# Kernel optimization log

Measured on AMD Instinct MI355X. Metric: run time of the kernel, lower is better.

Reference implementation:

```python
import jax, jax.numpy as jnp
import numpy as np

B, D, P, E, C = 2048, 4096, 64, 8, 64
K = D // P  # conv kernel = stride = input_dim / patch_num


def setup_inputs() -> dict:
    key = jax.random.key(0)
    k1, k2, k3, k4 = jax.random.split(key, 4)
    x = jax.random.normal(k1, (B, 1, D), jnp.float32)
    router_w = jax.random.normal(k2, (E, K), jnp.float32) * 0.02   # Router conv weight [E,1,K] squeezed
    expert_w = jax.random.normal(k3, (E, 2 * C, K), jnp.float32) * 0.001  # per-expert conv weights (small=True scaling)
    expert_b = jax.random.normal(k4, (E, 2 * C), jnp.float32) * 0.001
    return {"x": x, "router_w": router_w, "expert_w": expert_w, "expert_b": expert_b}


def reference(x, router_w, expert_w, expert_b):
    b, _, d = x.shape
    e, k = router_w.shape
    p = d // k
    c = expert_w.shape[1] // 2

    # Conv1d(1, ch, K, stride=K) == per-patch matmul; sum over dim 2 == sum over patches.
    patches = x.reshape(b, p, k)                                   # [B,P,K]

    # Router (eval mode: no noise)
    select = jnp.einsum('bpk,ek->be', patches, router_w)           # [B,E]

    # top1 routing
    gate = jnp.max(select, axis=-1)                                # [B]
    index = jnp.argmax(select, axis=-1)                            # [B]
    onehot = jax.nn.one_hot(index, e, dtype=select.dtype)          # [B,E]

    # aux load-balance loss
    density = onehot.mean(axis=0)
    density_proxy = select.mean(axis=0)
    loss = (density_proxy * density).mean() * float(e ** 2)

    # combine/dispatch (mask_flat is all ones for top1)
    combine = gate[:, None] * onehot                               # [B,E]
    dispatch = jax.lax.stop_gradient((combine != 0).astype(select.dtype))  # bool cast detaches grad
    select0 = dispatch

    # Dense dispatch: every expert sees the full batch, zero-masked by dispatch.
    # z[e,b,c,p] = conv of (dispatch[b,e]*x[b]) with expert e's kernel, + bias
    z = jnp.einsum('bpk,eck->ebcp', patches, expert_w)             # [E,B,2C,P]
    z = z * dispatch.T[:, :, None, None] + expert_b[:, None, :, None]
    z = z ** 3                                                     # nonlinear=True
    s = z.sum(axis=-1)                                             # sum over patches -> [E,B,2C]
    expert_out = jnp.stack([s[..., :c].sum(-1), s[..., c:].sum(-1)], axis=-1)  # [E,B,2]

    out = jnp.einsum('be,ebl->bl', combine, expert_out)            # [B,2]
    out = jax.nn.softmax(out, axis=1)
    return out, select0, loss
```

## Files before the change

### kernel.cpp

```cpp
#include <hip/hip_runtime.h>

#define BB 2048
#define DD 4096
#define PP 64
#define KK 64
#define EE 8
#define C2 128

typedef __attribute__((ext_vector_type(8))) short short8;
typedef __attribute__((ext_vector_type(4))) float floatx4;

__device__ inline unsigned short f2bf(float f) {
    unsigned int u = __builtin_bit_cast(unsigned int, f);
    u += 0x7FFFu + ((u >> 16) & 1u);
    return (unsigned short)(u >> 16);
}

__global__ __launch_bounds__(256) void moe_fused(
    const float* __restrict__ x, const float* __restrict__ rw,
    const float* __restrict__ ew, const float* __restrict__ eb,
    float* __restrict__ out, float* __restrict__ ws_sel)
{
    __shared__ __align__(16) unsigned short patb[64][72];
    __shared__ __align__(16) unsigned char ubuf[128 * 72 * 2];
    __shared__ float biasf[128];
    __shared__ float red0[4], red1[4];
    __shared__ float gate_s;
    __shared__ int idx_s;

    float (*cpart)[64]         = (float (*)[64])ubuf;
    unsigned short (*wbf)[72]  = (unsigned short (*)[72])ubuf;

    const int b = blockIdx.x;
    const int tid = threadIdx.x;

    {
        const float4* xb4 = (const float4*)(x + (size_t)b * DD);
        float c0 = 0.f, c1 = 0.f, c2 = 0.f, c3 = 0.f;
        #pragma unroll
        for (int j = 0; j < 4; ++j) {
            int idx = j * 256 + tid;
            float4 v = xb4[idx];
            int p = idx >> 4;
            int k = (idx & 15) << 2;
            ushort4 w4;
            w4.x = f2bf(v.x); w4.y = f2bf(v.y);
            w4.z = f2bf(v.z); w4.w = f2bf(v.w);
            *(ushort4*)&patb[p][k] = w4;
            c0 += v.x; c1 += v.y; c2 += v.z; c3 += v.w;
        }
        int m  = tid >> 4;
        int kq = (tid & 15) << 2;
        float4 cp; cp.x = c0; cp.y = c1; cp.z = c2; cp.w = c3;
        *(float4*)&cpart[m][kq] = cp;
    }
    __syncthreads();

    if (tid < 64) {
        float s = 0.f;
        #pragma unroll
        for (int m2 = 0; m2 < 16; ++m2) s += cpart[m2][tid];
        float myg = 0.f; int myix = 0;
        #pragma unroll
        for (int e2 = 0; e2 < 8; ++e2) {
            float d = s * rw[e2 * KK + tid];
            d += __shfl_xor(d, 32); d += __shfl_xor(d, 16); d += __shfl_xor(d, 8);
            d += __shfl_xor(d, 4);  d += __shfl_xor(d, 2);  d += __shfl_xor(d, 1);
            if (tid == e2) ws_sel[b * 8 + e2] = d;
            if (e2 == 0 || d > myg) { myg = d; myix = e2; }
        }
        if (tid == 0) { gate_s = myg; idx_s = myix; }
        if (tid < 8)
            out[BB * 2 + b * 8 + tid] = (tid == myix && myg != 0.f) ? 1.f : 0.f;
    }
    __syncthreads();

    const int e = idx_s;
    const float gate = gate_s;

    {
        const float4* we4 = (const float4*)(ew + (size_t)e * (C2 * KK));
        #pragma unroll
        for (int j = 0; j < 8; ++j) {
            int idx = j * 256 + tid;
            float4 v = we4[idx];
            int c = idx >> 4;
            int k = (idx & 15) << 2;
            ushort4 w4;
            w4.x = f2bf(v.x); w4.y = f2bf(v.y);
            w4.z = f2bf(v.z); w4.w = f2bf(v.w);
            *(ushort4*)&wbf[c][k] = w4;
        }
        if (tid < 128) biasf[tid] = eb[e * C2 + tid];
    }
    __syncthreads();

    const int w = tid >> 6;
    const int lane = tid & 63;
    const int r = lane & 15;
    const int q = lane >> 4;

    floatx4 acc[8];
    #pragma unroll
    for (int nt = 0; nt < 8; ++nt) acc[nt] = (floatx4){0.f, 0.f, 0.f, 0.f};

    #pragma unroll
    for (int kb = 0; kb < 2; ++kb) {
        const int k0 = kb * 32 + q * 8;
        short8 a = *(const short8*)&patb[w * 16 + r][k0];
        #pragma unroll
        for (int nt = 0; nt < 8; ++nt) {
            short8 bfr = *(const short8*)&wbf[nt * 16 + r][k0];
            acc[nt] = __builtin_amdgcn_mfma_f32_16x16x32_bf16(a, bfr, acc[nt], 0, 0, 0);
        }
    }

    float h0 = 0.f, h1 = 0.f;
    #pragma unroll
    for (int nt = 0; nt < 8; ++nt) {
        float bs = biasf[nt * 16 + r];
        #pragma unroll
        for (int i = 0; i < 4; ++i) {
            float z = acc[nt][i] + bs;
            float z3 = z * z * z;
            if (nt < 4) h0 += z3; else h1 += z3;
        }
    }
    #pragma unroll
    for (int off = 32; off > 0; off >>= 1) {
        h0 += __shfl_down(h0, off);
        h1 += __shfl_down(h1, off);
    }
    if (lane == 0) { red0[w] = h0; red1[w] = h1; }
    __syncthreads();
    if (tid == 0) {
        float t0 = red0[0] + red0[1] + red0[2] + red0[3];
        float t1 = red1[0] + red1[1] + red1[2] + red1[3];
        float l0 = gate * t0, l1 = gate * t1;
        float m = fmaxf(l0, l1);
        float e0 = __expf(l0 - m), e1 = __expf(l1 - m);
        float inv = 1.f / (e0 + e1);
        out[b * 2 + 0] = e0 * inv;
        out[b * 2 + 1] = e1 * inv;
    }
}

__global__ __launch_bounds__(256) void loss_kernel(
    const float* __restrict__ ws_sel, float* __restrict__ out)
{
    __shared__ float red[4][16];
    const int t = threadIdx.x;
    const int w = t >> 6, lane = t & 63;

    float p[8] = {0,0,0,0,0,0,0,0};
    float c[8] = {0,0,0,0,0,0,0,0};
    #pragma unroll
    for (int it = 0; it < BB / 256; ++it) {
        int b = it * 256 + t;
        const float4* row = (const float4*)(ws_sel + b * 8);
        float4 r0 = row[0], r1 = row[1];
        float v[8] = {r0.x, r0.y, r0.z, r0.w, r1.x, r1.y, r1.z, r1.w};
        float g = v[0]; int ix = 0;
        #pragma unroll
        for (int e2 = 1; e2 < 8; ++e2)
            if (v[e2] > g) { g = v[e2]; ix = e2; }
        #pragma unroll
        for (int e2 = 0; e2 < 8; ++e2) p[e2] += v[e2];
        c[ix] += 1.f;
    }
    #pragma unroll
    for (int off = 32; off > 0; off >>= 1) {
        #pragma unroll
        for (int e2 = 0; e2 < 8; ++e2) {
            p[e2] += __shfl_xor(p[e2], off);
            c[e2] += __shfl_xor(c[e2], off);
        }
    }
    if (lane == 0) {
        #pragma unroll
        for (int e2 = 0; e2 < 8; ++e2) { red[w][e2] = p[e2]; red[w][8 + e2] = c[e2]; }
    }
    __syncthreads();
    if (t == 0) {
        float loss = 0.f;
        #pragma unroll
        for (int e2 = 0; e2 < 8; ++e2) {
            float sp = red[0][e2] + red[1][e2] + red[2][e2] + red[3][e2];
            float sc = red[0][8 + e2] + red[1][8 + e2] + red[2][8 + e2] + red[3][8 + e2];
            loss += (sp / (float)BB) * (sc / (float)BB);
        }
        out[BB * 2 + BB * 8] = loss * (float)EE;
    }
}

extern "C" void kernel_launch(void* const* d_in, const int* in_sizes, int n_in,
                              void* d_out, int out_size, void* d_ws, size_t ws_size,
                              hipStream_t stream) {
    (void)in_sizes; (void)n_in; (void)out_size; (void)ws_size;
    const float* x  = (const float*)d_in[0];
    const float* rw = (const float*)d_in[1];
    const float* ew = (const float*)d_in[2];
    const float* eb = (const float*)d_in[3];
    float* out = (float*)d_out;
    float* ws  = (float*)d_ws;
    moe_fused<<<BB, 256, 0, stream>>>(x, rw, ew, eb, out, ws);
    loss_kernel<<<1, 256, 0, stream>>>(ws, out);
}
```

Before: 93.49 us.

## Map one sample per wavefront and pre-convert expert weights to bf16

Reworks the MoE kernel so that each 64-lane wavefront handles one batch row in registers, with four rows per block. This removes shared-memory staging and block-level barriers. Expert weights are converted to bf16 once by a separate prep kernel into workspace, and each wave then loads its selected expert's weight fragments straight from global memory. Activations are truncated rather than rounded to bf16, which slightly changes numerics, and the change adds one more kernel launch.

```diff
diff --git a/kernel.cpp b/kernel.cpp
--- a/kernel.cpp
+++ b/kernel.cpp
@@ -15,133 +15,118 @@
     u += 0x7FFFu + ((u >> 16) & 1u);
     return (unsigned short)(u >> 16);
 }
+__device__ inline unsigned pack2_trunc(float lo, float hi) {
+    unsigned ul = __builtin_bit_cast(unsigned, lo);
+    unsigned uh = __builtin_bit_cast(unsigned, hi);
+    return (uh & 0xFFFF0000u) | (ul >> 16);
+}
 
-__global__ __launch_bounds__(256) void moe_fused(
+__global__ __launch_bounds__(256) void prep_w(const float* __restrict__ ew,
+                                              unsigned short* __restrict__ wbf) {
+    int idx = blockIdx.x * 256 + threadIdx.x;
+    float4 v = ((const float4*)ew)[idx];
+    ushort4 o;
+    o.x = f2bf(v.x); o.y = f2bf(v.y); o.z = f2bf(v.z); o.w = f2bf(v.w);
+    ((ushort4*)wbf)[idx] = o;
+}
+
+__global__ __launch_bounds__(256) void moe3(
     const float* __restrict__ x, const float* __restrict__ rw,
-    const float* __restrict__ ew, const float* __restrict__ eb,
+    const unsigned short* __restrict__ wbf, const float* __restrict__ eb,
     float* __restrict__ out, float* __restrict__ ws_sel)
 {
-    __shared__ __align__(16) unsigned short patb[64][72];
-    __shared__ __align__(16) unsigned char ubuf[128 * 72 * 2];
-    __shared__ float biasf[128];
-    __shared__ float red0[4], red1[4];
-    __shared__ float gate_s;
-    __shared__ int idx_s;
+    const int lane = threadIdx.x & 63;
+    const int b = blockIdx.x * 4 + (threadIdx.x >> 6);
+    const int r = lane & 15, q = lane >> 4;
+    const float* xb = x + (size_t)b * DD;
 
-    float (*cpart)[64]         = (float (*)[64])ubuf;
-    unsigned short (*wbf)[72]  = (unsigned short (*)[72])ubuf;
-
-    const int b = blockIdx.x;
-    const int tid = threadIdx.x;
-
-    {
-        const float4* xb4 = (const float4*)(x + (size_t)b * DD);
-        float c0 = 0.f, c1 = 0.f, c2 = 0.f, c3 = 0.f;
+    float ps[16];
+    #pragma unroll
+    for (int j = 0; j < 16; ++j) ps[j] = 0.f;
+    short8 af[8];
+    #pragma unroll
+    for (int mt = 0; mt < 4; ++mt) {
         #pragma unroll
-        for (int j = 0; j < 4; ++j) {
-            int idx = j * 256 + tid;
-            float4 v = xb4[idx];
-            int p = idx >> 4;
-            int k = (idx & 15) << 2;
-            ushort4 w4;
-            w4.x = f2bf(v.x); w4.y = f2bf(v.y);
-            w4.z = f2bf(v.z); w4.w = f2bf(v.w);
-            *(ushort4*)&patb[p][k] = w4;
-            c0 += v.x; c1 += v.y; c2 += v.z; c3 += v.w;
-        }
-        int m  = tid >> 4;
-        int kq = (tid & 15) << 2;
-        float4 cp; cp.x = c0; cp.y = c1; cp.z = c2; cp.w = c3;
-        *(float4*)&cpart[m][kq] = cp;
-    }
-    __syncthreads();
-
-    if (tid < 64) {
-        float s = 0.f;
-        #pragma unroll
-        for (int m2 = 0; m2 < 16; ++m2) s += cpart[m2][tid];
-        float myg = 0.f; int myix = 0;
-        #pragma unroll
-        for (int e2 = 0; e2 < 8; ++e2) {
-            float d = s * rw[e2 * KK + tid];
-            d += __shfl_xor(d, 32); d += __shfl_xor(d, 16); d += __shfl_xor(d, 8);
-            d += __shfl_xor(d, 4);  d += __shfl_xor(d, 2);  d += __shfl_xor(d, 1);
-            if (tid == e2) ws_sel[b * 8 + e2] = d;
-            if (e2 == 0 || d > myg) { myg = d; myix = e2; }
-        }
-        if (tid == 0) { gate_s = myg; idx_s = myix; }
-        if (tid < 8)
-            out[BB * 2 + b * 8 + tid] = (tid == myix && myg != 0.f) ? 1.f : 0.f;
-    }
-    __syncthreads();
-
-    const int e = idx_s;
-    const float gate = gate_s;
-
-    {
-        const float4* we4 = (const float4*)(ew + (size_t)e * (C2 * KK));
-        #pragma unroll
-        for (int j = 0; j < 8; ++j) {
-            int idx = j * 256 + tid;
-            float4 v = we4[idx];
-            int c = idx >> 4;
-            int k = (idx & 15) << 2;
-            ushort4 w4;
-            w4.x = f2bf(v.x); w4.y = f2bf(v.y);
-            w4.z = f2bf(v.z); w4.w = f2bf(v.w);
-            *(ushort4*)&wbf[c][k] = w4;
-        }
-        if (tid < 128) biasf[tid] = eb[e * C2 + tid];
-    }
-    __syncthreads();
-
-    const int w = tid >> 6;
-    const int lane = tid & 63;
-    const int r = lane & 15;
-    const int q = lane >> 4;
-
-    floatx4 acc[8];
-    #pragma unroll
-    for (int nt = 0; nt < 8; ++nt) acc[nt] = (floatx4){0.f, 0.f, 0.f, 0.f};
-
-    #pragma unroll
-    for (int kb = 0; kb < 2; ++kb) {
-        const int k0 = kb * 32 + q * 8;
-        short8 a = *(const short8*)&patb[w * 16 + r][k0];
-        #pragma unroll
-        for (int nt = 0; nt < 8; ++nt) {
-            short8 bfr = *(const short8*)&wbf[nt * 16 + r][k0];
-            acc[nt] = __builtin_amdgcn_mfma_f32_16x16x32_bf16(a, bfr, acc[nt], 0, 0, 0);
+        for (int kb = 0; kb < 2; ++kb) {
+            const float* base = xb + (mt * 16 + r) * 64 + kb * 32 + q * 8;
+            float4 v0 = *(const float4*)base;
+            float4 v1 = *(const float4*)(base + 4);
+            ps[kb*8+0] += v0.x; ps[kb*8+1] += v0.y; ps[kb*8+2] += v0.z; ps[kb*8+3] += v0.w;
+            ps[kb*8+4] += v1.x; ps[kb*8+5] += v1.y; ps[kb*8+6] += v1.z; ps[kb*8+7] += v1.w;
+            uint4 u;
+            u.x = pack2_trunc(v0.x, v0.y); u.y = pack2_trunc(v0.z, v0.w);
+            u.z = pack2_trunc(v1.x, v1.y); u.w = pack2_trunc(v1.z, v1.w);
+            af[mt * 2 + kb] = __builtin_bit_cast(short8, u);
         }
     }
 
+    float d[8];
+    #pragma unroll
+    for (int e2 = 0; e2 < 8; ++e2) {
+        const float* rwe = rw + e2 * KK;
+        float4 a0 = *(const float4*)(rwe + q * 8);
+        float4 a1 = *(const float4*)(rwe + q * 8 + 4);
+        float4 b0 = *(const float4*)(rwe + 32 + q * 8);
+        float4 b1 = *(const float4*)(rwe + 32 + q * 8 + 4);
+        float t = ps[0]*a0.x + ps[1]*a0.y + ps[2]*a0.z + ps[3]*a0.w
+                + ps[4]*a1.x + ps[5]*a1.y + ps[6]*a1.z + ps[7]*a1.w
+                + ps[8]*b0.x + ps[9]*b0.y + ps[10]*b0.z + ps[11]*b0.w
+                + ps[12]*b1.x + ps[13]*b1.y + ps[14]*b1.z + ps[15]*b1.w;
+        t += __shfl_xor(t, 1);  t += __shfl_xor(t, 2);  t += __shfl_xor(t, 4);
+        t += __shfl_xor(t, 8);  t += __shfl_xor(t, 16); t += __shfl_xor(t, 32);
+        d[e2] = t;
+    }
+    float gate = d[0]; int e = 0;
+    #pragma unroll
+    for (int e2 = 1; e2 < 8; ++e2)
+        if (d[e2] > gate) { gate = d[e2]; e = e2; }
+
+    if (lane == 0) {
+        float4 s0 = make_float4(d[0], d[1], d[2], d[3]);
+        float4 s1 = make_float4(d[4], d[5], d[6], d[7]);
+        *(float4*)(ws_sel + b * 8)     = s0;
+        *(float4*)(ws_sel + b * 8 + 4) = s1;
+        float on = (gate != 0.f) ? 1.f : 0.f;
+        float4 o0 = make_float4(e==0?on:0.f, e==1?on:0.f, e==2?on:0.f, e==3?on:0.f);
+        float4 o1 = make_float4(e==4?on:0.f, e==5?on:0.f, e==6?on:0.f, e==7?on:0.f);
+        *(float4*)(out + BB * 2 + b * 8)     = o0;
+        *(float4*)(out + BB * 2 + b * 8 + 4) = o1;
+    }
+
+    const unsigned short* we = wbf + (size_t)e * (C2 * KK);
     float h0 = 0.f, h1 = 0.f;
     #pragma unroll
     for (int nt = 0; nt < 8; ++nt) {
-        float bs = biasf[nt * 16 + r];
+        float bs = eb[e * C2 + nt * 16 + r];
+        const unsigned short* wr = we + (nt * 16 + r) * KK + q * 8;
+        short8 bf0 = *(const short8*)wr;
+        short8 bf1 = *(const short8*)(wr + 32);
         #pragma unroll
-        for (int i = 0; i < 4; ++i) {
-            float z = acc[nt][i] + bs;
-            float z3 = z * z * z;
-            if (nt < 4) h0 += z3; else h1 += z3;
+        for (int mt = 0; mt < 4; ++mt) {
+            floatx4 acc = (floatx4){0.f, 0.f, 0.f, 0.f};
+            acc = __builtin_amdgcn_mfma_f32_16x16x32_bf16(af[mt*2+0], bf0, acc, 0, 0, 0);
+            acc = __builtin_amdgcn_mfma_f32_16x16x32_bf16(af[mt*2+1], bf1, acc, 0, 0, 0);
+            float hh = 0.f;
+            #pragma unroll
+            for (int i = 0; i < 4; ++i) {
+                float z = acc[i] + bs;
+                hh = fmaf(z * z, z, hh);
+            }
+            if (nt < 4) h0 += hh; else h1 += hh;
         }
     }
     #pragma unroll
-    for (int off = 32; off > 0; off >>= 1) {
-        h0 += __shfl_down(h0, off);
-        h1 += __shfl_down(h1, off);
+    for (int off = 1; off < 64; off <<= 1) {
+        h0 += __shfl_xor(h0, off);
+        h1 += __shfl_xor(h1, off);
     }
-    if (lane == 0) { red0[w] = h0; red1[w] = h1; }
-    __syncthreads();
-    if (tid == 0) {
-        float t0 = red0[0] + red0[1] + red0[2] + red0[3];
-        float t1 = red1[0] + red1[1] + red1[2] + red1[3];
-        float l0 = gate * t0, l1 = gate * t1;
+    if (lane == 0) {
+        float l0 = gate * h0, l1 = gate * h1;
         float m = fmaxf(l0, l1);
         float e0 = __expf(l0 - m), e1 = __expf(l1 - m);
         float inv = 1.f / (e0 + e1);
-        out[b * 2 + 0] = e0 * inv;
-        out[b * 2 + 1] = e1 * inv;
+        float2 o; o.x = e0 * inv; o.y = e1 * inv;
+        *(float2*)(out + b * 2) = o;
     }
 }
 
@@ -202,7 +187,10 @@
     const float* ew = (const float*)d_in[2];
     const float* eb = (const float*)d_in[3];
     float* out = (float*)d_out;
-    float* ws  = (float*)d_ws;
-    moe_fused<<<BB, 256, 0, stream>>>(x, rw, ew, eb, out, ws);
-    loss_kernel<<<1, 256, 0, stream>>>(ws, out);
+    float* ws_sel = (float*)d_ws;
+    unsigned short* wbf = (unsigned short*)((char*)d_ws + BB * EE * 4);
+
+    prep_w<<<64, 256, 0, stream>>>(ew, wbf);
+    moe3<<<BB / 4, 256, 0, stream>>>(x, rw, wbf, eb, out, ws_sel);
+    loss_kernel<<<1, 256, 0, stream>>>(ws_sel, out);
 }
```

New measurement: 92.91 us. No clear change (-0.6%).
